# Optimization experiments

Hardware: AMD Instinct MI355X
Metric: run time of the kernel (lower is better)

Reference implementation:

```python
import jax, jax.numpy as jnp
import numpy as np

N_NODES = 100000
NEG_SLOPE = 0.2  # PyG GATConv default negative_slope


def gat_layer(x, src, dst, W, a_src, a_dst, b):
    """PyG-style GATConv (eval mode: dropout = identity), concat=True.
    x: [N, F_in]; W: [F_in, H*C]; a_src/a_dst: [H, C]; b: [H*C].
    src/dst: [E] edge endpoints (messages flow src -> dst), self-loops included.
    """
    N = x.shape[0]
    H, C = a_src.shape
    h = (x @ W).reshape(N, H, C)                       # [N, H, C]
    al_s = jnp.sum(h * a_src, axis=-1)                 # [N, H]
    al_d = jnp.sum(h * a_dst, axis=-1)                 # [N, H]
    e = jax.nn.leaky_relu(al_s[src] + al_d[dst], NEG_SLOPE)  # [E, H]
    # softmax over incoming edges of each dst node (every node has a self-loop)
    m = jax.ops.segment_max(e, dst, num_segments=N)    # [N, H]
    ex = jnp.exp(e - m[dst])
    s = jax.ops.segment_sum(ex, dst, num_segments=N)   # [N, H]
    alpha = ex / s[dst]                                # [E, H]
    out = jax.ops.segment_sum(h[src] * alpha[:, :, None], dst, num_segments=N)
    return out.reshape(N, H * C) + b


def setup_inputs() -> dict:
    key = jax.random.key(0)
    ks = jax.random.split(key, 12)
    F_in, Hc, H, n_cls = 128, 32, 4, 3
    x = jax.random.normal(ks[0], (N_NODES, F_in), dtype=jnp.float32)
    edge_index = jax.random.randint(ks[1], (2, 1600000), 0, N_NODES, dtype=jnp.int64)
    sc1 = 1.0 / np.sqrt(F_in)
    sc2 = 1.0 / np.sqrt(Hc * H)
    return {
        "x": x,
        "edge_index": edge_index,
        "W1": jax.random.normal(ks[2], (F_in, H * Hc), dtype=jnp.float32) * sc1,
        "a1_src": jax.random.normal(ks[3], (H, Hc), dtype=jnp.float32) * sc1,
        "a1_dst": jax.random.normal(ks[4], (H, Hc), dtype=jnp.float32) * sc1,
        "b1": jnp.zeros((H * Hc,), dtype=jnp.float32),
        "W2": jax.random.normal(ks[5], (H * Hc, Hc), dtype=jnp.float32) * sc2,
        "a2_src": jax.random.normal(ks[6], (1, Hc), dtype=jnp.float32) * sc2,
        "a2_dst": jax.random.normal(ks[7], (1, Hc), dtype=jnp.float32) * sc2,
        "b2": jnp.zeros((Hc,), dtype=jnp.float32),
        "lin_W": jax.random.normal(ks[8], (Hc, n_cls), dtype=jnp.float32) * (1.0 / np.sqrt(Hc)),
        "lin_b": jnp.zeros((n_cls,), dtype=jnp.float32),
    }


def reference(x, edge_index, W1, a1_src, a1_dst, b1, W2, a2_src, a2_dst, b2, lin_W, lin_b):
    N = x.shape[0]
    loops = jnp.arange(N, dtype=edge_index.dtype)
    src = jnp.concatenate([edge_index[0], loops])
    dst = jnp.concatenate([edge_index[1], loops])
    h = jax.nn.elu(gat_layer(x, src, dst, W1, a1_src, a1_dst, b1))
    h = gat_layer(h, src, dst, W2, a2_src, a2_dst, b2)
    pooled = h.mean(axis=0, keepdims=True)             # batch=None path: [1, Hc]
    return jax.nn.softmax(pooled @ lin_W + lin_b, axis=1)
```

## Files before the change

kernel.cpp:

```cpp
#include <hip/hip_runtime.h>
#include <cstdint>
#include <cstddef>

static inline size_t align_up(size_t v, size_t a) { return (v + a - 1) & ~(a - 1); }

#define BCAP 3072

typedef __attribute__((ext_vector_type(8))) short short8;
typedef __attribute__((ext_vector_type(4))) float f32x4;
typedef __attribute__((ext_vector_type(2))) float f32x2;

__device__ inline unsigned short bf16_1(float x) {
  unsigned u = __float_as_uint(x);
  u += 0x7FFFu + ((u >> 16) & 1u);
  return (unsigned short)(u >> 16);
}
__device__ inline unsigned cvt_pk_bf16(float lo, float hi) {
  unsigned r;
  asm("v_cvt_pk_bf16_f32 %0, %1, %2" : "=v"(r) : "v"(lo), "v"(hi));
  return r;
}

__device__ inline unsigned char fp8_1(float x) {
  return (unsigned char)(__builtin_amdgcn_cvt_pk_fp8_f32(x, x, 0, false) & 0xFF);
}

__global__ void prep_kernel(const float* __restrict__ W1, const float* __restrict__ W2,
                            unsigned short* __restrict__ w1t, unsigned short* __restrict__ w2t,
                            int* __restrict__ fillB) {
  int t = blockIdx.x * 256 + threadIdx.x;
  if (t < 16384) {
    int c = t >> 7, k = t & 127;
    w1t[t] = bf16_1(W1[(size_t)k * 128 + c]);
  } else if (t < 20480) {
    int i = t - 16384;
    int c = i >> 7, k = i & 127;
    w2t[i] = bf16_1(W2[(size_t)k * 32 + c]);
  } else if (t < 21504) {
    fillB[t - 20480] = 0;
  }
}


__device__ inline int load_edge(const void* eidx, int is64, size_t idx) {
  if (is64) return (int)((const long long*)eidx)[idx];
  return ((const int*)eidx)[idx];
}

__global__ __launch_bounds__(256) void sortA_kernel(const void* eidx, int E,
                                                    int* __restrict__ fillB,
                                                    unsigned* __restrict__ packed, int NB) {
  __shared__ int hist[1024];
  __shared__ int loff[1024];
  __shared__ int lbase[1024];
  __shared__ int lcnt[1024];
  __shared__ unsigned sortedV[2048];
  __shared__ unsigned short sortedB[2048];
  __shared__ int s_is64;
  const int t = threadIdx.x;
  const int chunk0 = blockIdx.x * 2048;
  const int cntE = min(2048, E - chunk0);
  if (t == 0) s_is64 = 1;
  for (int i = t; i < 1024; i += 256) { hist[i] = 0; lcnt[i] = 0; }
  __syncthreads();
  {
    int nchk = min(cntE, 256);
    for (int i = t; i < nchk; i += 256)
      if (((const unsigned*)eidx)[2 * (size_t)(chunk0 + i) + 1] != 0u) s_is64 = 0;
  }
  __syncthreads();
  const int is64 = s_is64;
  int sv[8], dv[8];
#pragma unroll
  for (int it = 0; it < 8; ++it) {
    int li = it * 256 + t;
    if (li < cntE) {
      sv[it] = load_edge(eidx, is64, (size_t)chunk0 + li);
      dv[it] = load_edge(eidx, is64, (size_t)E + chunk0 + li);
      atomicAdd(&hist[dv[it] >> 7], 1);
    }
  }
  __syncthreads();
  for (int b = t; b < NB; b += 256) {
    int h = hist[b];
    if (h) lbase[b] = b * BCAP + atomicAdd(&fillB[b], h);
  }
  {
    int base = t * 4;
    int v[4]; int s = 0;
    __shared__ int sd[256];
#pragma unroll
    for (int j = 0; j < 4; ++j) { v[j] = hist[base + j]; s += v[j]; }
    sd[t] = s; __syncthreads();
    for (int off = 1; off < 256; off <<= 1) {
      int u = (t >= off) ? sd[t - off] : 0;
      __syncthreads();
      sd[t] += u;
      __syncthreads();
    }
    int run = sd[t] - s;
#pragma unroll
    for (int j = 0; j < 4; ++j) { loff[base + j] = run; run += v[j]; }
  }
  __syncthreads();
#pragma unroll
  for (int it = 0; it < 8; ++it) {
    int li = it * 256 + t;
    if (li < cntE) {
      int b = dv[it] >> 7;
      int r = atomicAdd(&lcnt[b], 1);
      int pos = loff[b] + r;
      sortedV[pos] = (unsigned)sv[it] | ((unsigned)(dv[it] & 127) << 20);
      sortedB[pos] = (unsigned short)b;
    }
  }
  __syncthreads();
  for (int li = t; li < cntE; li += 256) {
    int b = sortedB[li];
    packed[(size_t)lbase[b] + (li - loff[b])] = sortedV[li];
  }
}

__global__ __launch_bounds__(256) void buildCSR_kernel(const unsigned* __restrict__ packed,
                                                       const int* __restrict__ fillB,
                                                       int* __restrict__ rowbeg,
                                                       int* __restrict__ rowend,
                                                       int* __restrict__ csr, int N, int NB) {
  __shared__ int cnt[128], ex[128], fill[128];
  const int b = blockIdx.x;
  const int t = threadIdx.x;
  const int beg = b * BCAP;
  const int end = beg + fillB[b];
  const int node0 = b << 7;
  const int nn = min(128, N - node0);
  if (t < 128) { cnt[t] = 0; fill[t] = 0; }
  __syncthreads();
  for (int i = beg + t; i < end; i += 256) {
    int j = (packed[i] >> 20) & 127;
    atomicAdd(&cnt[j], 1);
  }
  __syncthreads();
  if (t < 128) ex[t] = cnt[t];
  __syncthreads();
  for (int off = 1; off < 128; off <<= 1) {
    int u = (t >= off && t < 128) ? ex[t - off] : 0;
    __syncthreads();
    if (t < 128) ex[t] += u;
    __syncthreads();
  }
  if (t < 128) ex[t] -= cnt[t];
  __syncthreads();
  if (t < nn) {
    rowbeg[node0 + t] = beg + ex[t];
    rowend[node0 + t] = beg + ex[t] + cnt[t];
  }
  for (int i = beg + t; i < end; i += 256) {
    unsigned v = packed[i];
    int j = (v >> 20) & 127;
    int r = atomicAdd(&fill[j], 1);
    csr[beg + ex[j] + r] = (int)(v & 0xFFFFFu);
  }
}

__global__ __launch_bounds__(256) void gemm1_mfma(
    const float* __restrict__ x, const unsigned short* __restrict__ w1t,
    const float* __restrict__ a1s, const float* __restrict__ a1d,
    unsigned char* __restrict__ h1f, float* __restrict__ al1s, float* __restrict__ al1d, int N) {
  __shared__ unsigned short sw[128 * 136];
  __shared__ unsigned short sx[64 * 136];
  unsigned char* ftile = (unsigned char*)sx;
  const int t = threadIdx.x;
  const int row0 = blockIdx.x * 64;
  for (int i = t; i < 4096; i += 256) {
    int c = i >> 5, k4 = (i & 31) * 4;
    *(ushort4*)&sw[c * 136 + k4] = *(const ushort4*)&w1t[c * 128 + k4];
  }
  for (int i = t; i < 2048; i += 256) {
    int r = i >> 5, c4 = (i & 31) * 4;
    float4 v = make_float4(0.f, 0.f, 0.f, 0.f);
    if (row0 + r < N) v = *(const float4*)(x + (size_t)(row0 + r) * 128 + c4);
    uint2 b;
    b.x = cvt_pk_bf16(v.x, v.y);
    b.y = cvt_pk_bf16(v.z, v.w);
    *(uint2*)&sx[r * 136 + c4] = b;
  }
  __syncthreads();
  const int lane = t & 63, wave = t >> 6;
  const int m = lane & 15, quad = lane >> 4;
  const unsigned short* arow = &sx[(wave * 16 + m) * 136];
  short8 A[4];
#pragma unroll
  for (int ks = 0; ks < 4; ++ks) A[ks] = *(const short8*)&arow[ks * 32 + quad * 8];
  __syncthreads();
  const int lrow = wave * 16 + quad * 4;
#pragma unroll
  for (int nt = 0; nt < 8; ++nt) {
    const unsigned short* brow = &sw[(nt * 16 + m) * 136];
    f32x4 acc = {0.f, 0.f, 0.f, 0.f};
#pragma unroll
    for (int ks = 0; ks < 4; ++ks) {
      short8 B = *(const short8*)&brow[ks * 32 + quad * 8];
      acc = __builtin_amdgcn_mfma_f32_16x16x32_bf16(A[ks], B, acc, 0, 0, 0);
    }
#pragma unroll
    for (int r = 0; r < 4; ++r)
      ftile[(lrow + r) * 128 + nt * 16 + m] = fp8_1(acc[r]);
  }
  __syncthreads();
#pragma unroll
  for (int it = 0; it < 2; ++it) {
    int row = it * 32 + (t >> 3);
    int chunk = t & 7;
    uint4 v = *(const uint4*)&ftile[row * 128 + chunk * 16];
    int grow = row0 + row;
    if (grow < N) *(uint4*)&h1f[(size_t)grow * 128 + chunk * 16] = v;
    unsigned w[4] = {v.x, v.y, v.z, v.w};
    float ps = 0.f, pd = 0.f;
    int cb = chunk * 16;
#pragma unroll
    for (int q = 0; q < 4; ++q) {
      f32x2 lo = __builtin_amdgcn_cvt_pk_f32_fp8((int)w[q], false);
      f32x2 hi = __builtin_amdgcn_cvt_pk_f32_fp8((int)w[q], true);
      int c = cb + q * 4;
      ps += lo[0] * a1s[c] + lo[1] * a1s[c + 1] + hi[0] * a1s[c + 2] + hi[1] * a1s[c + 3];
      pd += lo[0] * a1d[c] + lo[1] * a1d[c + 1] + hi[0] * a1d[c + 2] + hi[1] * a1d[c + 3];
    }
    ps += __shfl_xor(ps, 1); pd += __shfl_xor(pd, 1);
    if ((chunk & 1) == 0 && grow < N) {
      int head = chunk >> 1;
      al1s[(size_t)grow * 4 + head] = ps;
      al1d[(size_t)grow * 4 + head] = pd;
    }
  }
}

__global__ __launch_bounds__(256) void gemm2_mfma(
    const unsigned* __restrict__ houtb, const unsigned short* __restrict__ w2t,
    const float* __restrict__ a2s, const float* __restrict__ a2d,
    unsigned char* __restrict__ h2f, float* __restrict__ al2s, float* __restrict__ al2d, int N) {
  __shared__ unsigned short sw[32 * 136];
  __shared__ unsigned short sx[64 * 136];
  unsigned char* ftile = (unsigned char*)sx;
  const int t = threadIdx.x;
  const int row0 = blockIdx.x * 64;
  for (int i = t; i < 1024; i += 256) {
    int c = i >> 5, k4 = (i & 31) * 4;
    *(ushort4*)&sw[c * 136 + k4] = *(const ushort4*)&w2t[c * 128 + k4];
  }
  for (int i = t; i < 2048; i += 256) {
    int r = i >> 5, d2 = (i & 31) * 2;
    uint2 v = make_uint2(0u, 0u);
    if (row0 + r < N) v = *(const uint2*)(houtb + (size_t)(row0 + r) * 64 + d2);
    *(uint2*)&sx[r * 136 + d2 * 2] = v;
  }
  __syncthreads();
  const int lane = t & 63, wave = t >> 6;
  const int m = lane & 15, quad = lane >> 4;
  const unsigned short* arow = &sx[(wave * 16 + m) * 136];
  short8 A[4];
#pragma unroll
  for (int ks = 0; ks < 4; ++ks) A[ks] = *(const short8*)&arow[ks * 32 + quad * 8];
  __syncthreads();
  const int lrow = wave * 16 + quad * 4;
#pragma unroll
  for (int nt = 0; nt < 2; ++nt) {
    const unsigned short* brow = &sw[(nt * 16 + m) * 136];
    f32x4 acc = {0.f, 0.f, 0.f, 0.f};
#pragma unroll
    for (int ks = 0; ks < 4; ++ks) {
      short8 B = *(const short8*)&brow[ks * 32 + quad * 8];
      acc = __builtin_amdgcn_mfma_f32_16x16x32_bf16(A[ks], B, acc, 0, 0, 0);
    }
#pragma unroll
    for (int r = 0; r < 4; ++r)
      ftile[(lrow + r) * 32 + nt * 16 + m] = fp8_1(acc[r]);
  }
  __syncthreads();
  if (t < 128) {
    int row = t >> 1, chunk = t & 1;
    uint4 v = *(const uint4*)&ftile[row * 32 + chunk * 16];
    int grow = row0 + row;
    if (grow < N) *(uint4*)&h2f[(size_t)grow * 32 + chunk * 16] = v;
    unsigned w[4] = {v.x, v.y, v.z, v.w};
    float ps = 0.f, pd = 0.f;
    int cb = chunk * 16;
#pragma unroll
    for (int q = 0; q < 4; ++q) {
      f32x2 lo = __builtin_amdgcn_cvt_pk_f32_fp8((int)w[q], false);
      f32x2 hi = __builtin_amdgcn_cvt_pk_f32_fp8((int)w[q], true);
      int c = cb + q * 4;
      ps += lo[0] * a2s[c] + lo[1] * a2s[c + 1] + hi[0] * a2s[c + 2] + hi[1] * a2s[c + 3];
      pd += lo[0] * a2d[c] + lo[1] * a2d[c + 1] + hi[0] * a2d[c + 2] + hi[1] * a2d[c + 3];
    }
    ps += __shfl_xor(ps, 1); pd += __shfl_xor(pd, 1);
    if (chunk == 0 && grow < N) { al2s[grow] = ps; al2d[grow] = pd; }
  }
}

#define DEC8P(HV, EX)                                                       \
  {                                                                         \
    f32x2 _e2; _e2[0] = (EX); _e2[1] = (EX);                                \
    acc01 += __builtin_amdgcn_cvt_pk_f32_fp8((int)(HV).x, false) * _e2;     \
    acc23 += __builtin_amdgcn_cvt_pk_f32_fp8((int)(HV).x, true) * _e2;      \
    acc45 += __builtin_amdgcn_cvt_pk_f32_fp8((int)(HV).y, false) * _e2;     \
    acc67 += __builtin_amdgcn_cvt_pk_f32_fp8((int)(HV).y, true) * _e2;      \
    den += (EX);                                                            \
  }

__global__ __launch_bounds__(256) void agg1_kernel(
    const int* __restrict__ rowbeg, const int* __restrict__ rowend, const int* __restrict__ csr_src,
    const unsigned char* __restrict__ h1f,
    const float* __restrict__ al_s, const float* __restrict__ al_d,
    const float* __restrict__ b1, unsigned* __restrict__ houtb, int N) {
  int t = threadIdx.x;
  int d = (blockIdx.x * 256 + t) >> 6;
  if (d >= N) return;
  int lane = t & 63;
  int e_id = lane >> 4;
  unsigned c8 = (unsigned)(lane & 15);
  unsigned head = c8 >> 2;
  const unsigned boff = c8 * 8u;
  const float ald = al_d[(unsigned)d * 4u + head];
  const int beg = __builtin_amdgcn_readfirstlane(rowbeg[d]);
  const int end = __builtin_amdgcn_readfirstlane(rowend[d]);
  int idx0 = beg + e_id;
  int idx1 = idx0 + 4;
  int sj0 = (idx0 < end) ? csr_src[(unsigned)idx0] : d;
  int sj1 = (idx1 < end) ? csr_src[(unsigned)idx1] : d;
  float self_as = al_s[(unsigned)d * 4u + head];
  uint2 self_hv = *(const uint2*)(h1f + (((unsigned)d << 7) | boff));
  idx0 += 8; idx1 += 8;
  int nsj0 = (idx0 < end) ? csr_src[(unsigned)idx0] : d;
  int nsj1 = (idx1 < end) ? csr_src[(unsigned)idx1] : d;
  float as0 = al_s[(unsigned)sj0 * 4u + head];
  float as1 = al_s[(unsigned)sj1 * 4u + head];
  uint2 hv0 = *(const uint2*)(h1f + (((unsigned)sj0 << 7) | boff));
  uint2 hv1 = *(const uint2*)(h1f + (((unsigned)sj1 << 7) | boff));
  f32x2 acc01 = {0.f, 0.f}, acc23 = {0.f, 0.f}, acc45 = {0.f, 0.f}, acc67 = {0.f, 0.f};
  float den = 0.f;
  {
    float e = self_as + ald;
    e = fmaxf(e, 0.2f * e);
    float ex = (e_id == 0) ? __expf(e) : 0.f;
    DEC8P(self_hv, ex);
  }
  for (int i = beg; i < end; i += 8) {
    idx0 += 8; idx1 += 8;
    int nnsj0 = (idx0 < end) ? csr_src[(unsigned)idx0] : d;
    int nnsj1 = (idx1 < end) ? csr_src[(unsigned)idx1] : d;
    float nas0 = al_s[(unsigned)nsj0 * 4u + head];
    float nas1 = al_s[(unsigned)nsj1 * 4u + head];
    uint2 nhv0 = *(const uint2*)(h1f + (((unsigned)nsj0 << 7) | boff));
    uint2 nhv1 = *(const uint2*)(h1f + (((unsigned)nsj1 << 7) | boff));
    int cix0 = i + e_id;
    int cix1 = cix0 + 4;
    float e0 = as0 + ald;
    e0 = fmaxf(e0, 0.2f * e0);
    float ex0 = __expf(e0);
    if (cix0 >= end) ex0 = 0.f;
    float e1 = as1 + ald;
    e1 = fmaxf(e1, 0.2f * e1);
    float ex1 = __expf(e1);
    if (cix1 >= end) ex1 = 0.f;
    DEC8P(hv0, ex0);
    DEC8P(hv1, ex1);
    as0 = nas0; as1 = nas1; hv0 = nhv0; hv1 = nhv1;
    nsj0 = nnsj0; nsj1 = nnsj1;
  }
  float a0 = acc01[0], a1 = acc01[1], a2 = acc23[0], a3 = acc23[1];
  float a4 = acc45[0], a5 = acc45[1], a6 = acc67[0], a7 = acc67[1];
  a0 += __shfl_xor(a0, 16); a1 += __shfl_xor(a1, 16);
  a2 += __shfl_xor(a2, 16); a3 += __shfl_xor(a3, 16);
  a4 += __shfl_xor(a4, 16); a5 += __shfl_xor(a5, 16);
  a6 += __shfl_xor(a6, 16); a7 += __shfl_xor(a7, 16);
  den += __shfl_xor(den, 16);
  a0 += __shfl_xor(a0, 32); a1 += __shfl_xor(a1, 32);
  a2 += __shfl_xor(a2, 32); a3 += __shfl_xor(a3, 32);
  a4 += __shfl_xor(a4, 32); a5 += __shfl_xor(a5, 32);
  a6 += __shfl_xor(a6, 32); a7 += __shfl_xor(a7, 32);
  den += __shfl_xor(den, 32);
  float inv = __builtin_amdgcn_rcpf(den);
  float p0 = e_id == 0 ? a0 : e_id == 1 ? a2 : e_id == 2 ? a4 : a6;
  float p1 = e_id == 0 ? a1 : e_id == 1 ? a3 : e_id == 2 ? a5 : a7;
  float2 bv = *(const float2*)(b1 + 8 * c8 + 2 * e_id);
  float o0 = p0 * inv + bv.x;
  float o1 = p1 * inv + bv.y;
  o0 = o0 > 0.f ? o0 : __expf(o0) - 1.f;
  o1 = o1 > 0.f ? o1 : __expf(o1) - 1.f;
  houtb[(unsigned)d * 64u + 4u * c8 + (unsigned)e_id] = cvt_pk_bf16(o0, o1);
}

__global__ __launch_bounds__(256) void agg2_kernel(
    const int* __restrict__ rowbeg, const int* __restrict__ rowend, const int* __restrict__ csr_src,
    const unsigned char* __restrict__ h2f,
    const float* __restrict__ al_s, const float* __restrict__ al_d,
    float* __restrict__ partial, int N) {
  __shared__ float sp[16 * 32];
  int t = threadIdx.x;
  int l16 = t & 15;
  int slot = t >> 4;
  int node = (blockIdx.x * 256 + t) >> 4;
  int e_id = l16 >> 2;
  unsigned c8 = (unsigned)(l16 & 3);
  const unsigned boff = c8 * 8u;
  float po0 = 0.f, po1 = 0.f;
  if (node < N) {
    const float ald = al_d[node];
    const int beg = rowbeg[node], end = rowend[node];
    int idx0 = beg + e_id;
    int idx1 = idx0 + 4;
    int sj0 = (idx0 < end) ? csr_src[(unsigned)idx0] : node;
    int sj1 = (idx1 < end) ? csr_src[(unsigned)idx1] : node;
    float self_as = al_s[node];
    uint2 self_hv = *(const uint2*)(h2f + (((unsigned)node << 5) | boff));
    idx0 += 8; idx1 += 8;
    int nsj0 = (idx0 < end) ? csr_src[(unsigned)idx0] : node;
    int nsj1 = (idx1 < end) ? csr_src[(unsigned)idx1] : node;
    float as0 = al_s[(unsigned)sj0];
    float as1 = al_s[(unsigned)sj1];
    uint2 hv0 = *(const uint2*)(h2f + (((unsigned)sj0 << 5) | boff));
    uint2 hv1 = *(const uint2*)(h2f + (((unsigned)sj1 << 5) | boff));
    f32x2 acc01 = {0.f, 0.f}, acc23 = {0.f, 0.f}, acc45 = {0.f, 0.f}, acc67 = {0.f, 0.f};
    float den = 0.f;
    {
      float e = self_as + ald;
      e = fmaxf(e, 0.2f * e);
      float ex = (e_id == 0) ? __expf(e) : 0.f;
      DEC8P(self_hv, ex);
    }
    for (int i = beg; i < end; i += 8) {
      idx0 += 8; idx1 += 8;
      int nnsj0 = (idx0 < end) ? csr_src[(unsigned)idx0] : node;
      int nnsj1 = (idx1 < end) ? csr_src[(unsigned)idx1] : node;
      float nas0 = al_s[(unsigned)nsj0];
      float nas1 = al_s[(unsigned)nsj1];
      uint2 nhv0 = *(const uint2*)(h2f + (((unsigned)nsj0 << 5) | boff));
      uint2 nhv1 = *(const uint2*)(h2f + (((unsigned)nsj1 << 5) | boff));
      int cix0 = i + e_id;
      int cix1 = cix0 + 4;
      float e0 = as0 + ald;
      e0 = fmaxf(e0, 0.2f * e0);
      float ex0 = __expf(e0);
      if (cix0 >= end) ex0 = 0.f;
      float e1 = as1 + ald;
      e1 = fmaxf(e1, 0.2f * e1);
      float ex1 = __expf(e1);
      if (cix1 >= end) ex1 = 0.f;
      DEC8P(hv0, ex0);
      DEC8P(hv1, ex1);
      as0 = nas0; as1 = nas1; hv0 = nhv0; hv1 = nhv1;
      nsj0 = nnsj0; nsj1 = nnsj1;
    }
    float a0 = acc01[0], a1 = acc01[1], a2 = acc23[0], a3 = acc23[1];
    float a4 = acc45[0], a5 = acc45[1], a6 = acc67[0], a7 = acc67[1];
    a0 += __shfl_xor(a0, 4); a1 += __shfl_xor(a1, 4);
    a2 += __shfl_xor(a2, 4); a3 += __shfl_xor(a3, 4);
    a4 += __shfl_xor(a4, 4); a5 += __shfl_xor(a5, 4);
    a6 += __shfl_xor(a6, 4); a7 += __shfl_xor(a7, 4);
    den += __shfl_xor(den, 4);
    a0 += __shfl_xor(a0, 8); a1 += __shfl_xor(a1, 8);
    a2 += __shfl_xor(a2, 8); a3 += __shfl_xor(a3, 8);
    a4 += __shfl_xor(a4, 8); a5 += __shfl_xor(a5, 8);
    a6 += __shfl_xor(a6, 8); a7 += __shfl_xor(a7, 8);
    den += __shfl_xor(den, 8);
    float inv = __builtin_amdgcn_rcpf(den);
    float p0 = e_id == 0 ? a0 : e_id == 1 ? a2 : e_id == 2 ? a4 : a6;
    float p1 = e_id == 0 ? a1 : e_id == 1 ? a3 : e_id == 2 ? a5 : a7;
    po0 = p0 * inv; po1 = p1 * inv;
  }
  *(float2*)&sp[slot * 32 + 8 * c8 + 2 * e_id] = make_float2(po0, po1);
  __syncthreads();
  if (t < 32) {
    float s = 0.f;
#pragma unroll
    for (int j = 0; j < 16; ++j) s += sp[j * 32 + t];
    partial[(size_t)blockIdx.x * 32 + t] = s;
  }
}

__global__ __launch_bounds__(256) void reduce_kernel(
    const float* __restrict__ partial, int nb, float* __restrict__ partial2) {
  __shared__ float sp[8 * 32];
  int t = threadIdx.x;
  int slot = t >> 5, c = t & 31;
  int row0 = blockIdx.x * 8 + slot;
  float s = 0.f;
  for (int i = row0; i < nb; i += 1024) s += partial[(size_t)i * 32 + c];
  sp[slot * 32 + c] = s;
  __syncthreads();
  if (t < 32) {
    float tot = 0.f;
#pragma unroll
    for (int j = 0; j < 8; ++j) tot += sp[j * 32 + t];
    partial2[(size_t)blockIdx.x * 32 + t] = tot;
  }
}

__global__ void final_kernel(const float* __restrict__ partial2, int nb,
                             const float* __restrict__ b2, const float* __restrict__ linW,
                             const float* __restrict__ linb, float* __restrict__ out, int N) {
  __shared__ float sd[256];
  __shared__ float pooled[32];
  int t = threadIdx.x;
  int c = t & 31, g = t >> 5;
  float s = 0.f;
  for (int i = g; i < nb; i += 8) s += partial2[(size_t)i * 32 + c];
  sd[t] = s; __syncthreads();
  if (t < 32) {
    float tot = 0.f;
#pragma unroll
    for (int j = 0; j < 8; ++j) tot += sd[j * 32 + t];
    pooled[t] = tot / (float)N + b2[t];
  }
  __syncthreads();
  if (t == 0) {
    float lg[3];
    for (int j = 0; j < 3; ++j) lg[j] = linb[j];
    for (int cc = 0; cc < 32; ++cc)
      for (int j = 0; j < 3; ++j) lg[j] += pooled[cc] * linW[cc * 3 + j];
    float m = fmaxf(lg[0], fmaxf(lg[1], lg[2]));
    float e0 = __expf(lg[0] - m), e1 = __expf(lg[1] - m), e2 = __expf(lg[2] - m);
    float inv = 1.f / (e0 + e1 + e2);
    out[0] = e0 * inv; out[1] = e1 * inv; out[2] = e2 * inv;
  }
}

extern "C" void kernel_launch(void* const* d_in, const int* in_sizes, int n_in,
                              void* d_out, int out_size, void* d_ws, size_t ws_size,
                              hipStream_t stream) {
  const float* x    = (const float*)d_in[0];
  const void*  eidx = d_in[1];
  const float* W1   = (const float*)d_in[2];
  const float* a1s  = (const float*)d_in[3];
  const float* a1d  = (const float*)d_in[4];
  const float* b1   = (const float*)d_in[5];
  const float* W2   = (const float*)d_in[6];
  const float* a2s  = (const float*)d_in[7];
  const float* a2d  = (const float*)d_in[8];
  const float* b2   = (const float*)d_in[9];
  const float* linW = (const float*)d_in[10];
  const float* linb = (const float*)d_in[11];
  float* out = (float*)d_out;

  const int N = in_sizes[0] / 128;
  const int E = in_sizes[1] / 2;
  const int NB = (N + 127) >> 7;

  char* ws = (char*)d_ws;
  size_t off = 0;
  auto alloc = [&](size_t bytes) -> void* {
    size_t o = off;
    off = align_up(off + bytes, 256);
    return (void*)(ws + o);
  };
  int* fillB  = (int*)alloc((size_t)1024 * sizeof(int));
  int* rowbeg = (int*)alloc((size_t)N * sizeof(int));
  int* rowend = (int*)alloc((size_t)N * sizeof(int));
  unsigned* packed = (unsigned*)alloc((size_t)NB * BCAP * sizeof(unsigned));
  int* csr    = (int*)alloc((size_t)NB * BCAP * sizeof(int));
  float* al1s = (float*)alloc((size_t)N * 4 * sizeof(float));
  float* al1d = (float*)alloc((size_t)N * 4 * sizeof(float));
  float* al2s = (float*)alloc((size_t)N * sizeof(float));
  float* al2d = (float*)alloc((size_t)N * sizeof(float));
  unsigned short* w1t = (unsigned short*)alloc(16384 * sizeof(unsigned short));
  unsigned short* w2t = (unsigned short*)alloc(4096 * sizeof(unsigned short));
  unsigned char* h1f  = (unsigned char*)alloc((size_t)N * 128);
  unsigned* houtb = (unsigned*)alloc((size_t)N * 64 * sizeof(unsigned));
  unsigned char* h2f  = (unsigned char*)alloc((size_t)N * 32);
  const int nAggBlocks = (N + 15) / 16;
  float* partial  = (float*)alloc((size_t)nAggBlocks * 32 * sizeof(float));
  float* partial2 = (float*)alloc((size_t)128 * 32 * sizeof(float));

  prep_kernel<<<84, 256, 0, stream>>>(W1, W2, w1t, w2t, fillB);

  sortA_kernel<<<(E + 2047) / 2048, 256, 0, stream>>>(eidx, E, fillB, packed, NB);
  buildCSR_kernel<<<NB, 256, 0, stream>>>(packed, fillB, rowbeg, rowend, csr, N, NB);

  const int gemmBlocks = (N + 63) / 64;
  gemm1_mfma<<<gemmBlocks, 256, 0, stream>>>(x, w1t, a1s, a1d, h1f, al1s, al1d, N);
  agg1_kernel<<<(N * 64 + 255) / 256, 256, 0, stream>>>(
      rowbeg, rowend, csr, h1f, al1s, al1d, b1, houtb, N);
  gemm2_mfma<<<gemmBlocks, 256, 0, stream>>>(houtb, w2t, a2s, a2d, h2f, al2s, al2d, N);
  agg2_kernel<<<(N * 16 + 255) / 256, 256, 0, stream>>>(
      rowbeg, rowend, csr, h2f, al2s, al2d, partial, N);
  reduce_kernel<<<128, 256, 0, stream>>>(partial, nAggBlocks, partial2);
  final_kernel<<<1, 256, 0, stream>>>(partial2, 128, b2, linW, linb, out, N);
}
```

Before: 266.8 us.

## Shorten agg1 gather prefetch depth and merge final reduction into one kernel

```diff
diff --git a/kernel.cpp b/kernel.cpp
--- a/kernel.cpp
+++ b/kernel.cpp
@@ -327,45 +327,35 @@
   int idx1 = idx0 + 4;
   int sj0 = (idx0 < end) ? csr_src[(unsigned)idx0] : d;
   int sj1 = (idx1 < end) ? csr_src[(unsigned)idx1] : d;
-  float self_as = al_s[(unsigned)d * 4u + head];
-  uint2 self_hv = *(const uint2*)(h1f + (((unsigned)d << 7) | boff));
-  idx0 += 8; idx1 += 8;
-  int nsj0 = (idx0 < end) ? csr_src[(unsigned)idx0] : d;
-  int nsj1 = (idx1 < end) ? csr_src[(unsigned)idx1] : d;
-  float as0 = al_s[(unsigned)sj0 * 4u + head];
-  float as1 = al_s[(unsigned)sj1 * 4u + head];
-  uint2 hv0 = *(const uint2*)(h1f + (((unsigned)sj0 << 7) | boff));
-  uint2 hv1 = *(const uint2*)(h1f + (((unsigned)sj1 << 7) | boff));
   f32x2 acc01 = {0.f, 0.f}, acc23 = {0.f, 0.f}, acc45 = {0.f, 0.f}, acc67 = {0.f, 0.f};
   float den = 0.f;
   {
-    float e = self_as + ald;
+    float e = al_s[(unsigned)d * 4u + head] + ald;
     e = fmaxf(e, 0.2f * e);
     float ex = (e_id == 0) ? __expf(e) : 0.f;
-    DEC8P(self_hv, ex);
+    uint2 hv = *(const uint2*)(h1f + (((unsigned)d << 7) | boff));
+    DEC8P(hv, ex);
   }
   for (int i = beg; i < end; i += 8) {
+    const int cidx0 = idx0, cidx1 = idx1;
+    const int csj0 = sj0, csj1 = sj1;
+    float as0 = al_s[(unsigned)csj0 * 4u + head];
+    float as1 = al_s[(unsigned)csj1 * 4u + head];
+    uint2 hv0 = *(const uint2*)(h1f + (((unsigned)csj0 << 7) | boff));
+    uint2 hv1 = *(const uint2*)(h1f + (((unsigned)csj1 << 7) | boff));
     idx0 += 8; idx1 += 8;
-    int nnsj0 = (idx0 < end) ? csr_src[(unsigned)idx0] : d;
-    int nnsj1 = (idx1 < end) ? csr_src[(unsigned)idx1] : d;
-    float nas0 = al_s[(unsigned)nsj0 * 4u + head];
-    float nas1 = al_s[(unsigned)nsj1 * 4u + head];
-    uint2 nhv0 = *(const uint2*)(h1f + (((unsigned)nsj0 << 7) | boff));
-    uint2 nhv1 = *(const uint2*)(h1f + (((unsigned)nsj1 << 7) | boff));
-    int cix0 = i + e_id;
-    int cix1 = cix0 + 4;
+    sj0 = (idx0 < end) ? csr_src[(unsigned)idx0] : d;
+    sj1 = (idx1 < end) ? csr_src[(unsigned)idx1] : d;
     float e0 = as0 + ald;
     e0 = fmaxf(e0, 0.2f * e0);
     float ex0 = __expf(e0);
-    if (cix0 >= end) ex0 = 0.f;
+    if (cidx0 >= end) ex0 = 0.f;
     float e1 = as1 + ald;
     e1 = fmaxf(e1, 0.2f * e1);
     float ex1 = __expf(e1);
-    if (cix1 >= end) ex1 = 0.f;
+    if (cidx1 >= end) ex1 = 0.f;
     DEC8P(hv0, ex0);
     DEC8P(hv1, ex1);
-    as0 = nas0; as1 = nas1; hv0 = nhv0; hv1 = nhv1;
-    nsj0 = nnsj0; nsj1 = nnsj1;
   }
   float a0 = acc01[0], a1 = acc01[1], a2 = acc23[0], a3 = acc23[1];
   float a4 = acc45[0], a5 = acc45[1], a6 = acc67[0], a7 = acc67[1];
@@ -478,38 +468,21 @@
   }
 }
 
-__global__ __launch_bounds__(256) void reduce_kernel(
-    const float* __restrict__ partial, int nb, float* __restrict__ partial2) {
-  __shared__ float sp[8 * 32];
-  int t = threadIdx.x;
-  int slot = t >> 5, c = t & 31;
-  int row0 = blockIdx.x * 8 + slot;
-  float s = 0.f;
-  for (int i = row0; i < nb; i += 1024) s += partial[(size_t)i * 32 + c];
-  sp[slot * 32 + c] = s;
-  __syncthreads();
-  if (t < 32) {
-    float tot = 0.f;
-#pragma unroll
-    for (int j = 0; j < 8; ++j) tot += sp[j * 32 + t];
-    partial2[(size_t)blockIdx.x * 32 + t] = tot;
-  }
-}
-
-__global__ void final_kernel(const float* __restrict__ partial2, int nb,
-                             const float* __restrict__ b2, const float* __restrict__ linW,
-                             const float* __restrict__ linb, float* __restrict__ out, int N) {
-  __shared__ float sd[256];
+__global__ __launch_bounds__(1024) void final_kernel(
+    const float* __restrict__ partial, int nb,
+    const float* __restrict__ b2, const float* __restrict__ linW,
+    const float* __restrict__ linb, float* __restrict__ out, int N) {
+  __shared__ float sd[1024];
   __shared__ float pooled[32];
   int t = threadIdx.x;
   int c = t & 31, g = t >> 5;
   float s = 0.f;
-  for (int i = g; i < nb; i += 8) s += partial2[(size_t)i * 32 + c];
+  for (int i = g; i < nb; i += 32) s += partial[(size_t)i * 32 + c];
   sd[t] = s; __syncthreads();
   if (t < 32) {
     float tot = 0.f;
 #pragma unroll
-    for (int j = 0; j < 8; ++j) tot += sd[j * 32 + t];
+    for (int j = 0; j < 32; ++j) tot += sd[j * 32 + t];
     pooled[t] = tot / (float)N + b2[t];
   }
   __syncthreads();
@@ -569,7 +542,6 @@
   unsigned char* h2f  = (unsigned char*)alloc((size_t)N * 32);
   const int nAggBlocks = (N + 15) / 16;
   float* partial  = (float*)alloc((size_t)nAggBlocks * 32 * sizeof(float));
-  float* partial2 = (float*)alloc((size_t)128 * 32 * sizeof(float));
 
   prep_kernel<<<84, 256, 0, stream>>>(W1, W2, w1t, w2t, fillB);
 
@@ -583,6 +555,5 @@
   gemm2_mfma<<<gemmBlocks, 256, 0, stream>>>(houtb, w2t, a2s, a2d, h2f, al2s, al2d, N);
   agg2_kernel<<<(N * 16 + 255) / 256, 256, 0, stream>>>(
       rowbeg, rowend, csr, h2f, al2s, al2d, partial, N);
-  reduce_kernel<<<128, 256, 0, stream>>>(partial, nAggBlocks, partial2);
-  final_kernel<<<1, 256, 0, stream>>>(partial2, 128, b2, linW, linb, out, N);
-}
+  final_kernel<<<1, 1024, 0, stream>>>(partial, nAggBlocks, b2, linW, linb, out, N);
+}
```

Result: slower. 305.9 us (+14.7%).
